# Kernel optimization log

Measured on AMD Instinct MI355X. Metric: run time of the kernel, lower is better.

## Reference

```python
import jax, jax.numpy as jnp
import numpy as np

V = 50000
D = 128
EF = 16
E = 800000
LN_EPS = 1e-5


def setup_inputs() -> dict:
    key = jax.random.key(0)
    ks = jax.random.split(key, 9)
    h = jax.random.normal(ks[0], (V, D), dtype=jnp.float32)
    edge_index = jax.random.randint(ks[1], (2, E), 0, V, dtype=jnp.int64)
    edge_attr = jax.random.normal(ks[2], (E, EF), dtype=jnp.float32)
    # msg_mlp = Linear(D+EF, D) -> ReLU -> Dropout(0) -> Linear(D, D)
    s1 = 1.0 / np.sqrt(D + EF)
    s2 = 1.0 / np.sqrt(D)
    W1 = jax.random.uniform(ks[3], (D + EF, D), minval=-s1, maxval=s1, dtype=jnp.float32)
    b1 = jax.random.uniform(ks[4], (D,), minval=-s1, maxval=s1, dtype=jnp.float32)
    W2 = jax.random.uniform(ks[5], (D, D), minval=-s2, maxval=s2, dtype=jnp.float32)
    b2 = jax.random.uniform(ks[6], (D,), minval=-s2, maxval=s2, dtype=jnp.float32)
    gamma = jnp.ones((D,), dtype=jnp.float32)
    beta = jnp.zeros((D,), dtype=jnp.float32)
    return {"h": h, "edge_index": edge_index, "edge_attr": edge_attr,
            "W1": W1, "b1": b1, "W2": W2, "b2": b2,
            "gamma": gamma, "beta": beta}


def _layer_norm(x, gamma, beta):
    mu = jnp.mean(x, axis=-1, keepdims=True)
    var = jnp.mean(jnp.square(x - mu), axis=-1, keepdims=True)
    return (x - mu) * jax.lax.rsqrt(var + LN_EPS) * gamma + beta


def reference(h, edge_index, edge_attr, W1, b1, W2, b2, gamma, beta):
    src, dst = edge_index[0], edge_index[1]
    # gather source node features, concat edge features: [E, D+EF]
    x = jnp.concatenate([h[src], edge_attr], axis=-1)
    # per-edge message MLP (dropout p=0 -> identity)
    msg = jax.nn.relu(x @ W1 + b1) @ W2 + b2  # [E, D]
    # scatter-add messages to destinations
    agg = jax.ops.segment_sum(msg, dst, num_segments=V)  # [V, D]
    # count initialized to ones BEFORE scatter_add -> denominator = 1 + in_degree
    deg = jax.ops.segment_sum(jnp.ones((E,), dtype=h.dtype), dst, num_segments=V)
    count = (1.0 + deg)[:, None]  # [V, 1]
    return _layer_norm(h + agg / count, gamma, beta)
```

## Files before the change

### kernel.cpp

```cpp
#include <hip/hip_runtime.h>
#include <hip/hip_bf16.h>

#define V 50000
#define D 128
#define EF 16
#define E_EDGES 800000
#define NT 12500
#define XSTR 168
#define YSTR 136
#define CSTR 132
#define NSCAN 196
#define EGRID 1024

typedef __attribute__((ext_vector_type(8))) __bf16 bf16x8;
typedef __attribute__((ext_vector_type(4))) float f32x4;

__device__ inline unsigned short f2bf(float f) {
    unsigned u = __float_as_uint(f);
    u += 0x7FFF + ((u >> 16) & 1);
    return (unsigned short)(u >> 16);
}
__device__ inline unsigned pack2(float a, float b) {
    return (unsigned)f2bf(a) | ((unsigned)f2bf(b) << 16);
}

__global__ __launch_bounds__(256)
void setup_kernel(const float* __restrict__ h, unsigned short* __restrict__ hbf,
                  const int* __restrict__ ei, int* __restrict__ cnt,
                  float* __restrict__ agg,
                  const float* __restrict__ W1, const float* __restrict__ W2,
                  unsigned short* __restrict__ W1p, unsigned short* __restrict__ W2p) {
    int idx = blockIdx.x * 256 + threadIdx.x;
    const float4 v = *(const float4*)(h + ((size_t)idx << 2));
    unsigned* o = (unsigned*)hbf + (idx << 1);
    o[0] = pack2(v.x, v.y);
    o[1] = pack2(v.z, v.w);
    *(float4*)(agg + ((size_t)idx << 2)) = (float4){0.f, 0.f, 0.f, 0.f};
    if (idx < E_EDGES) atomicAdd(&cnt[ei[E_EDGES + idx]], 1);
    if (idx < 5 * 128 * 32) {
        int kb = idx >> 12, rem = idx & 4095;
        int n = rem >> 5, kk = rem & 31;
        int k = kb * 32 + kk;
        W1p[idx] = f2bf((k < D + EF) ? W1[k * D + n] : 0.0f);
    }
    if (idx < 4 * 128 * 32) {
        int kb = idx >> 12, rem = idx & 4095;
        int n = rem >> 5, kk = rem & 31;
        W2p[idx] = f2bf(W2[(kb * 32 + kk) * D + n]);
    }
}

__device__ inline int block_excl_scan(int x, int t, int* ws) {
    int lane = t & 63, w = t >> 6;
    int inc = x;
    #pragma unroll
    for (int off = 1; off < 64; off <<= 1) {
        int y = __shfl_up(inc, off);
        if (lane >= off) inc += y;
    }
    if (lane == 63) ws[w] = inc;
    __syncthreads();
    if (t == 0) {
        int r = 0;
        #pragma unroll
        for (int i = 0; i < 4; ++i) { int c = ws[i]; ws[i] = r; r += c; }
    }
    __syncthreads();
    return inc - x + ws[w];
}

__global__ __launch_bounds__(256)
void scan1_kernel(const int* __restrict__ cnt, int* __restrict__ cursor,
                  int* __restrict__ bsum) {
    __shared__ int ws[4];
    __shared__ int tot;
    int t = threadIdx.x;
    int i = blockIdx.x * 256 + t;
    int x = (i < V) ? cnt[i] : 0;
    int ex = block_excl_scan(x, t, ws);
    if (i < V) cursor[i] = ex;
    if (t == 255) tot = ex + x;
    __syncthreads();
    if (t == 0) bsum[blockIdx.x] = tot;
}

__global__ __launch_bounds__(256)
void scatter_kernel(const int* __restrict__ ei, int* __restrict__ cursor,
                    const int* __restrict__ bsum,
                    int* __restrict__ srcs, int* __restrict__ dsts,
                    int* __restrict__ eidx) {
    __shared__ int ws[4];
    __shared__ int sboff[NSCAN];
    int t = threadIdx.x;
    int x = (t < NSCAN) ? bsum[t] : 0;
    int ex = block_excl_scan(x, t, ws);
    if (t < NSCAN) sboff[t] = ex;
    __syncthreads();
    int e = blockIdx.x * 256 + t;
    int d = ei[E_EDGES + e];
    int pos = atomicAdd(&cursor[d], 1) + sboff[d >> 8];
    srcs[pos] = ei[e];
    dsts[pos] = d;
    eidx[pos] = e;
}

__global__ __launch_bounds__(256, 3)
void edge_kernel(const unsigned short* __restrict__ hbf,
                 const float* __restrict__ ea,
                 const int* __restrict__ srcs, const int* __restrict__ dsts,
                 const int* __restrict__ eidx,
                 const unsigned short* __restrict__ W1p, const unsigned short* __restrict__ W2p,
                 const float* __restrict__ b1, const float* __restrict__ b2,
                 float* __restrict__ agg) {
    union SharedU {
        struct { unsigned short Xs[64 * XSTR]; unsigned short Ys[64 * YSTR]; } s;
        float C[64 * CSTR];
    };
    __shared__ __align__(16) SharedU u;
    __shared__ int sDst[64];

    const int tid  = threadIdx.x;
    const int lane = tid & 63;
    const int wave = tid >> 6;
    const int nlo  = lane & 15;
    const int kq   = lane >> 4;
    const int er   = tid >> 4;
    const int ec   = tid & 15;
    const int ee   = tid >> 2;
    const int eq   = tid & 3;

    bf16x8 B1[5][2], B2[4][2];
    float b1v[2], b2v[2];
    #pragma unroll
    for (int t = 0; t < 2; ++t) {
        int n = wave * 32 + t * 16 + nlo;
        b1v[t] = b1[n];
        b2v[t] = b2[n];
        #pragma unroll
        for (int kb = 0; kb < 5; ++kb)
            B1[kb][t] = *(const bf16x8*)(W1p + ((kb << 7) + n) * 32 + (kq << 3));
        #pragma unroll
        for (int kb = 0; kb < 4; ++kb)
            B2[kb][t] = *(const bf16x8*)(W2p + ((kb << 7) + n) * 32 + (kq << 3));
    }

    const int base0 = blockIdx.x << 6;
    int a0 = srcs[base0 + er];
    int a1 = srcs[base0 + er + 16];
    int a2 = srcs[base0 + er + 32];
    int a3 = srcs[base0 + er + 48];
    int aev = eidx[base0 + ee];
    int ddcur = dsts[base0 + lane];
    bf16x8 pf0 = *(const bf16x8*)(hbf + (size_t)a0 * D + (ec << 3));
    bf16x8 pf1 = *(const bf16x8*)(hbf + (size_t)a1 * D + (ec << 3));
    bf16x8 pf2 = *(const bf16x8*)(hbf + (size_t)a2 * D + (ec << 3));
    bf16x8 pf3 = *(const bf16x8*)(hbf + (size_t)a3 * D + (ec << 3));
    float4 pfe = *(const float4*)(ea + (size_t)aev * EF + (eq << 2));

    int n1 = blockIdx.x + EGRID;
    int nb1 = (n1 < NT ? n1 : blockIdx.x) << 6;
    int i1s0 = srcs[nb1 + er];
    int i1s1 = srcs[nb1 + er + 16];
    int i1s2 = srcs[nb1 + er + 32];
    int i1s3 = srcs[nb1 + er + 48];
    int i1e  = eidx[nb1 + ee];
    int i1d  = dsts[nb1 + lane];

    for (int tile = blockIdx.x; tile < NT; tile += EGRID) {
        int n2 = tile + 2 * EGRID;
        int nb2 = (n2 < NT ? n2 : tile) << 6;
        int i2s0 = srcs[nb2 + er];
        int i2s1 = srcs[nb2 + er + 16];
        int i2s2 = srcs[nb2 + er + 32];
        int i2s3 = srcs[nb2 + er + 48];
        int i2e  = eidx[nb2 + ee];
        int i2d  = dsts[nb2 + lane];

        if (tid < 64) sDst[tid] = ddcur;
        *(bf16x8*)(u.s.Xs + er * XSTR + (ec << 3))        = pf0;
        *(bf16x8*)(u.s.Xs + (er + 16) * XSTR + (ec << 3)) = pf1;
        *(bf16x8*)(u.s.Xs + (er + 32) * XSTR + (ec << 3)) = pf2;
        *(bf16x8*)(u.s.Xs + (er + 48) * XSTR + (ec << 3)) = pf3;
        {
            unsigned* xp = (unsigned*)(u.s.Xs) + ee * (XSTR / 2) + 64 + (eq << 1);
            xp[0] = pack2(pfe.x, pfe.y);
            xp[1] = pack2(pfe.z, pfe.w);
        }
        {
            int i0 = tid, i1 = tid + 256;
            ((unsigned*)(u.s.Xs))[(i0 >> 3) * (XSTR / 2) + 72 + (i0 & 7)] = 0u;
            ((unsigned*)(u.s.Xs))[(i1 >> 3) * (XSTR / 2) + 72 + (i1 & 7)] = 0u;
        }
        __syncthreads();

        bf16x8 q0 = *(const bf16x8*)(hbf + (size_t)i1s0 * D + (ec << 3));
        bf16x8 q1 = *(const bf16x8*)(hbf + (size_t)i1s1 * D + (ec << 3));
        bf16x8 q2 = *(const bf16x8*)(hbf + (size_t)i1s2 * D + (ec << 3));
        bf16x8 q3 = *(const bf16x8*)(hbf + (size_t)i1s3 * D + (ec << 3));
        float4 qe = *(const float4*)(ea + (size_t)i1e * EF + (eq << 2));
        int nextdd = i1d;

        f32x4 acc[4][2];
        #pragma unroll
        for (int mt = 0; mt < 4; ++mt)
            #pragma unroll
            for (int t = 0; t < 2; ++t)
                acc[mt][t] = (f32x4){0.f, 0.f, 0.f, 0.f};

        #pragma unroll
        for (int kb = 0; kb < 5; ++kb) {
            bf16x8 A[4];
            int ko = kb * 32 + (kq << 3);
            #pragma unroll
            for (int mt = 0; mt < 4; ++mt)
                A[mt] = *(const bf16x8*)(u.s.Xs + (mt * 16 + nlo) * XSTR + ko);
            #pragma unroll
            for (int mt = 0; mt < 4; ++mt)
                #pragma unroll
                for (int t = 0; t < 2; ++t)
                    acc[mt][t] = __builtin_amdgcn_mfma_f32_16x16x32_bf16(A[mt], B1[kb][t], acc[mt][t], 0, 0, 0);
        }

        #pragma unroll
        for (int mt = 0; mt < 4; ++mt)
            #pragma unroll
            for (int t = 0; t < 2; ++t)
                #pragma unroll
                for (int r = 0; r < 4; ++r) {
                    float v = fmaxf(acc[mt][t][r] + b1v[t], 0.0f);
                    int row = mt * 16 + (kq << 2) + r;
                    int col = wave * 32 + t * 16 + nlo;
                    u.s.Ys[row * YSTR + col] = f2bf(v);
                }
        __syncthreads();

        f32x4 acc2[4][2];
        #pragma unroll
        for (int mt = 0; mt < 4; ++mt)
            #pragma unroll
            for (int t = 0; t < 2; ++t)
                acc2[mt][t] = (f32x4){0.f, 0.f, 0.f, 0.f};

        #pragma unroll
        for (int kb = 0; kb < 4; ++kb) {
            bf16x8 A[4];
            int ko = kb * 32 + (kq << 3);
            #pragma unroll
            for (int mt = 0; mt < 4; ++mt)
                A[mt] = *(const bf16x8*)(u.s.Ys + (mt * 16 + nlo) * YSTR + ko);
            #pragma unroll
            for (int mt = 0; mt < 4; ++mt)
                #pragma unroll
                for (int t = 0; t < 2; ++t)
                    acc2[mt][t] = __builtin_amdgcn_mfma_f32_16x16x32_bf16(A[mt], B2[kb][t], acc2[mt][t], 0, 0, 0);
        }
        __syncthreads();

        #pragma unroll
        for (int mt = 0; mt < 4; ++mt)
            #pragma unroll
            for (int t = 0; t < 2; ++t)
                #pragma unroll
                for (int r = 0; r < 4; ++r) {
                    int row = mt * 16 + (kq << 2) + r;
                    int col = wave * 32 + t * 16 + nlo;
                    u.C[row * CSTR + col] = acc2[mt][t][r] + b2v[t];
                }
        __syncthreads();

        {
            int col = tid & 127;
            int rbase = (tid >> 7) << 5;
            float sum = 0.f;
            int cur = sDst[rbase];
            for (int i = 0; i < 32; ++i) {
                int row = rbase + i;
                int d = sDst[row];
                if (d != cur) {
                    atomicAdd(&agg[(size_t)cur * D + col], sum);
                    sum = 0.f;
                    cur = d;
                }
                sum += u.C[row * CSTR + col];
            }
            atomicAdd(&agg[(size_t)cur * D + col], sum);
        }
        __syncthreads();

        pf0 = q0; pf1 = q1; pf2 = q2; pf3 = q3; pfe = qe; ddcur = nextdd;
        i1s0 = i2s0; i1s1 = i2s1; i1s2 = i2s2; i1s3 = i2s3; i1e = i2e; i1d = i2d;
    }
}

__global__ __launch_bounds__(256)
void finalize_kernel(const float* __restrict__ h, const float* __restrict__ agg,
                     const int* __restrict__ cnt,
                     const float* __restrict__ gamma, const float* __restrict__ beta,
                     float* __restrict__ out) {
    int wave = threadIdx.x >> 6, lane = threadIdx.x & 63;
    int v = blockIdx.x * 4 + wave;
    if (v >= V) return;
    float inv = 1.0f / (1.0f + (float)cnt[v]);
    const float* hr = h + (size_t)v * D;
    const float* ar = agg + (size_t)v * D;
    float x0 = hr[lane]      + ar[lane]      * inv;
    float x1 = hr[lane + 64] + ar[lane + 64] * inv;
    float s = x0 + x1;
    #pragma unroll
    for (int m = 32; m; m >>= 1) s += __shfl_xor(s, m);
    float mu = s * (1.0f / 128.0f);
    float d0 = x0 - mu, d1 = x1 - mu;
    float vs = d0 * d0 + d1 * d1;
    #pragma unroll
    for (int m = 32; m; m >>= 1) vs += __shfl_xor(vs, m);
    float rs = rsqrtf(vs * (1.0f / 128.0f) + 1e-5f);
    out[(size_t)v * D + lane]      = d0 * rs * gamma[lane]      + beta[lane];
    out[(size_t)v * D + 64 + lane] = d1 * rs * gamma[lane + 64] + beta[lane + 64];
}

extern "C" void kernel_launch(void* const* d_in, const int* in_sizes, int n_in,
                              void* d_out, int out_size, void* d_ws, size_t ws_size,
                              hipStream_t stream) {
    const float* h     = (const float*)d_in[0];
    const int*   ei    = (const int*)d_in[1];
    const float* ea    = (const float*)d_in[2];
    const float* W1    = (const float*)d_in[3];
    const float* b1    = (const float*)d_in[4];
    const float* W2    = (const float*)d_in[5];
    const float* b2    = (const float*)d_in[6];
    const float* gamma = (const float*)d_in[7];
    const float* beta  = (const float*)d_in[8];
    float* out = (float*)d_out;

    char* ws = (char*)d_ws;
    float*          agg    = (float*)ws;
    int*            cnt    = (int*)(ws + 25600000);
    int*            cursor = (int*)(ws + 25800000);
    int*            bsum   = (int*)(ws + 26000000);
    int*            srcs   = (int*)(ws + 26000800);
    int*            dsts   = (int*)(ws + 29200800);
    int*            eidx   = (int*)(ws + 32400800);
    unsigned short* W1p    = (unsigned short*)(ws + 35600800);
    unsigned short* W2p    = (unsigned short*)(ws + 35641760);
    unsigned short* hbf    = (unsigned short*)(ws + 35674528);

    hipMemsetAsync(cnt, 0, 200000, stream);
    setup_kernel<<<6250, 256, 0, stream>>>(h, hbf, ei, cnt, agg, W1, W2, W1p, W2p);
    scan1_kernel<<<NSCAN, 256, 0, stream>>>(cnt, cursor, bsum);
    scatter_kernel<<<3125, 256, 0, stream>>>(ei, cursor, bsum, srcs, dsts, eidx);
    edge_kernel<<<EGRID, 256, 0, stream>>>(hbf, ea, srcs, dsts, eidx, W1p, W2p, b1, b2, agg);
    finalize_kernel<<<12500, 256, 0, stream>>>(h, agg, cnt, gamma, beta, out);
}
```

Before: 376.1 us.

## Precompute per-node h@W1 once and gather projected rows per edge

Uses linearity to compute U = h @ W1[:128] once per node (50k rows) in a new GEMM kernel instead of once per edge (800k), so each edge only computes the small edge-feature part (K=32) and adds the gathered U row before ReLU. This removes most of the first-layer MFMA work and shrinks the shared staging buffer, allowing occupancy to rise from 3 to 4 blocks per CU. The cost is an extra kernel launch plus a bf16 rounding of U before adding the edge term, which changes numerics slightly.

New measurement: 319.8 us. 1.18x faster.

```diff
diff --git a/kernel.cpp b/kernel.cpp
--- a/kernel.cpp
+++ b/kernel.cpp
@@ -6,11 +6,12 @@
 #define EF 16
 #define E_EDGES 800000
 #define NT 12500
-#define XSTR 168
-#define YSTR 136
+#define USTR 136
+#define XESTR 40
 #define CSTR 132
 #define NSCAN 196
 #define EGRID 1024
+#define UGRID 782
 
 typedef __attribute__((ext_vector_type(8))) __bf16 bf16x8;
 typedef __attribute__((ext_vector_type(4))) float f32x4;
@@ -23,18 +24,16 @@
 __device__ inline unsigned pack2(float a, float b) {
     return (unsigned)f2bf(a) | ((unsigned)f2bf(b) << 16);
 }
+__device__ inline float bf2f(unsigned short u) {
+    return __uint_as_float((unsigned)u << 16);
+}
 
 __global__ __launch_bounds__(256)
-void setup_kernel(const float* __restrict__ h, unsigned short* __restrict__ hbf,
-                  const int* __restrict__ ei, int* __restrict__ cnt,
+void setup_kernel(const int* __restrict__ ei, int* __restrict__ cnt,
                   float* __restrict__ agg,
                   const float* __restrict__ W1, const float* __restrict__ W2,
                   unsigned short* __restrict__ W1p, unsigned short* __restrict__ W2p) {
     int idx = blockIdx.x * 256 + threadIdx.x;
-    const float4 v = *(const float4*)(h + ((size_t)idx << 2));
-    unsigned* o = (unsigned*)hbf + (idx << 1);
-    o[0] = pack2(v.x, v.y);
-    o[1] = pack2(v.z, v.w);
     *(float4*)(agg + ((size_t)idx << 2)) = (float4){0.f, 0.f, 0.f, 0.f};
     if (idx < E_EDGES) atomicAdd(&cnt[ei[E_EDGES + idx]], 1);
     if (idx < 5 * 128 * 32) {
@@ -48,6 +47,80 @@
         int n = rem >> 5, kk = rem & 31;
         W2p[idx] = f2bf(W2[(kb * 32 + kk) * D + n]);
     }
+}
+
+__global__ __launch_bounds__(256)
+void u_gemm_kernel(const float* __restrict__ h,
+                   const unsigned short* __restrict__ W1p,
+                   unsigned short* __restrict__ U) {
+    __shared__ __align__(16) unsigned short Hs[64 * USTR];
+    const int tid  = threadIdx.x;
+    const int lane = tid & 63;
+    const int wave = tid >> 6;
+    const int nlo  = lane & 15;
+    const int kq   = lane >> 4;
+    const int er   = tid >> 4;
+    const int ec   = tid & 15;
+    const int gbase = blockIdx.x << 6;
+
+    bf16x8 B1[4][2];
+    #pragma unroll
+    for (int t = 0; t < 2; ++t) {
+        int n = wave * 32 + t * 16 + nlo;
+        #pragma unroll
+        for (int kb = 0; kb < 4; ++kb)
+            B1[kb][t] = *(const bf16x8*)(W1p + ((kb << 7) + n) * 32 + (kq << 3));
+    }
+
+    #pragma unroll
+    for (int m = 0; m < 4; ++m) {
+        int row = er + m * 16;
+        int grow = gbase + row;
+        unsigned* o = (unsigned*)(Hs + row * USTR + (ec << 3));
+        if (grow < V) {
+            const float4* p = (const float4*)(h + (size_t)grow * D + (ec << 3));
+            float4 v0 = p[0], v1 = p[1];
+            o[0] = pack2(v0.x, v0.y); o[1] = pack2(v0.z, v0.w);
+            o[2] = pack2(v1.x, v1.y); o[3] = pack2(v1.z, v1.w);
+        } else {
+            o[0] = 0u; o[1] = 0u; o[2] = 0u; o[3] = 0u;
+        }
+    }
+    __syncthreads();
+
+    f32x4 acc[4][2];
+    #pragma unroll
+    for (int mt = 0; mt < 4; ++mt)
+        #pragma unroll
+        for (int t = 0; t < 2; ++t)
+            acc[mt][t] = (f32x4){0.f, 0.f, 0.f, 0.f};
+
+    #pragma unroll
+    for (int kb = 0; kb < 4; ++kb) {
+        bf16x8 A[4];
+        int ko = kb * 32 + (kq << 3);
+        #pragma unroll
+        for (int mt = 0; mt < 4; ++mt)
+            A[mt] = *(const bf16x8*)(Hs + (mt * 16 + nlo) * USTR + ko);
+        #pragma unroll
+        for (int mt = 0; mt < 4; ++mt)
+            #pragma unroll
+            for (int t = 0; t < 2; ++t)
+                acc[mt][t] = __builtin_amdgcn_mfma_f32_16x16x32_bf16(A[mt], B1[kb][t], acc[mt][t], 0, 0, 0);
+    }
+
+    #pragma unroll
+    for (int mt = 0; mt < 4; ++mt)
+        #pragma unroll
+        for (int t = 0; t < 2; ++t)
+            #pragma unroll
+            for (int r = 0; r < 4; ++r) {
+                int row = mt * 16 + (kq << 2) + r;
+                int grow = gbase + row;
+                int col = wave * 32 + t * 16 + nlo;
+                if (grow < V)
+                    U[(size_t)grow * D + col] = f2bf(acc[mt][t][r]);
+            }
 }
 
 __device__ inline int block_excl_scan(int x, int t, int* ws) {
@@ -104,8 +177,8 @@
     eidx[pos] = e;
 }
 
-__global__ __launch_bounds__(256, 3)
-void edge_kernel(const unsigned short* __restrict__ hbf,
+__global__ __launch_bounds__(256, 4)
+void edge_kernel(const unsigned short* __restrict__ U,
                  const float* __restrict__ ea,
                  const int* __restrict__ srcs, const int* __restrict__ dsts,
                  const int* __restrict__ eidx,
@@ -113,10 +186,11 @@
                  const float* __restrict__ b1, const float* __restrict__ b2,
                  float* __restrict__ agg) {
     union SharedU {
-        struct { unsigned short Xs[64 * XSTR]; unsigned short Ys[64 * YSTR]; } s;
+        unsigned short Us[64 * USTR];
         float C[64 * CSTR];
     };
     __shared__ __align__(16) SharedU u;
+    __shared__ __align__(16) unsigned short Xe[64 * XESTR];
     __shared__ int sDst[64];
 
     const int tid  = threadIdx.x;
@@ -129,19 +203,24 @@
     const int ee   = tid >> 2;
     const int eq   = tid & 3;
 
-    bf16x8 B1[5][2], B2[4][2];
+    bf16x8 B1e[2], B2[4][2];
     float b1v[2], b2v[2];
     #pragma unroll
     for (int t = 0; t < 2; ++t) {
         int n = wave * 32 + t * 16 + nlo;
         b1v[t] = b1[n];
         b2v[t] = b2[n];
-        #pragma unroll
-        for (int kb = 0; kb < 5; ++kb)
-            B1[kb][t] = *(const bf16x8*)(W1p + ((kb << 7) + n) * 32 + (kq << 3));
+        B1e[t] = *(const bf16x8*)(W1p + ((4 << 7) + n) * 32 + (kq << 3));
         #pragma unroll
         for (int kb = 0; kb < 4; ++kb)
             B2[kb][t] = *(const bf16x8*)(W2p + ((kb << 7) + n) * 32 + (kq << 3));
+    }
+
+    {
+        unsigned* xz = (unsigned*)Xe;
+        int i0 = tid, i1 = tid + 256;
+        xz[(i0 >> 3) * (XESTR / 2) + 8 + (i0 & 7)] = 0u;
+        xz[(i1 >> 3) * (XESTR / 2) + 8 + (i1 & 7)] = 0u;
     }
 
     const int base0 = blockIdx.x << 6;
@@ -151,10 +230,10 @@
     int a3 = srcs[base0 + er + 48];
     int aev = eidx[base0 + ee];
     int ddcur = dsts[base0 + lane];
-    bf16x8 pf0 = *(const bf16x8*)(hbf + (size_t)a0 * D + (ec << 3));
-    bf16x8 pf1 = *(const bf16x8*)(hbf + (size_t)a1 * D + (ec << 3));
-    bf16x8 pf2 = *(const bf16x8*)(hbf + (size_t)a2 * D + (ec << 3));
-    bf16x8 pf3 = *(const bf16x8*)(hbf + (size_t)a3 * D + (ec << 3));
+    bf16x8 pf0 = *(const bf16x8*)(U + (size_t)a0 * D + (ec << 3));
+    bf16x8 pf1 = *(const bf16x8*)(U + (size_t)a1 * D + (ec << 3));
+    bf16x8 pf2 = *(const bf16x8*)(U + (size_t)a2 * D + (ec << 3));
+    bf16x8 pf3 = *(const bf16x8*)(U + (size_t)a3 * D + (ec << 3));
     float4 pfe = *(const float4*)(ea + (size_t)aev * EF + (eq << 2));
 
     int n1 = blockIdx.x + EGRID;
@@ -177,48 +256,40 @@
         int i2d  = dsts[nb2 + lane];
 
         if (tid < 64) sDst[tid] = ddcur;
-        *(bf16x8*)(u.s.Xs + er * XSTR + (ec << 3))        = pf0;
-        *(bf16x8*)(u.s.Xs + (er + 16) * XSTR + (ec << 3)) = pf1;
-        *(bf16x8*)(u.s.Xs + (er + 32) * XSTR + (ec << 3)) = pf2;
-        *(bf16x8*)(u.s.Xs + (er + 48) * XSTR + (ec << 3)) = pf3;
+        *(bf16x8*)(u.Us + er * USTR + (ec << 3))        = pf0;
+        *(bf16x8*)(u.Us + (er + 16) * USTR + (ec << 3)) = pf1;
+        *(bf16x8*)(u.Us + (er + 32) * USTR + (ec << 3)) = pf2;
+        *(bf16x8*)(u.Us + (er + 48) * USTR + (ec << 3)) = pf3;
         {
-            unsigned* xp = (unsigned*)(u.s.Xs) + ee * (XSTR / 2) + 64 + (eq << 1);
+            unsigned* xp = (unsigned*)Xe + ee * (XESTR / 2) + (eq << 1);
             xp[0] = pack2(pfe.x, pfe.y);
             xp[1] = pack2(pfe.z, pfe.w);
         }
-        {
-            int i0 = tid, i1 = tid + 256;
-            ((unsigned*)(u.s.Xs))[(i0 >> 3) * (XSTR / 2) + 72 + (i0 & 7)] = 0u;
-            ((unsigned*)(u.s.Xs))[(i1 >> 3) * (XSTR / 2) + 72 + (i1 & 7)] = 0u;
-        }
         __syncthreads();
 
-        bf16x8 q0 = *(const bf16x8*)(hbf + (size_t)i1s0 * D + (ec << 3));
-        bf16x8 q1 = *(const bf16x8*)(hbf + (size_t)i1s1 * D + (ec << 3));
-        bf16x8 q2 = *(const bf16x8*)(hbf + (size_t)i1s2 * D + (ec << 3));
-        bf16x8 q3 = *(const bf16x8*)(hbf + (size_t)i1s3 * D + (ec << 3));
+        bf16x8 q0 = *(const bf16x8*)(U + (size_t)i1s0 * D + (ec << 3));
+        bf16x8 q1 = *(const bf16x8*)(U + (size_t)i1s1 * D + (ec << 3));
+        bf16x8 q2 = *(const bf16x8*)(U + (size_t)i1s2 * D + (ec << 3));
+        bf16x8 q3 = *(const bf16x8*)(U + (size_t)i1s3 * D + (ec << 3));
         float4 qe = *(const float4*)(ea + (size_t)i1e * EF + (eq << 2));
         int nextdd = i1d;
 
-        f32x4 acc[4][2];
+        f32x4 accE[4][2];
         #pragma unroll
         for (int mt = 0; mt < 4; ++mt)
             #pragma unroll
             for (int t = 0; t < 2; ++t)
-                acc[mt][t] = (f32x4){0.f, 0.f, 0.f, 0.f};
-
-        #pragma unroll
-        for (int kb = 0; kb < 5; ++kb) {
+                accE[mt][t] = (f32x4){0.f, 0.f, 0.f, 0.f};
+        {
             bf16x8 A[4];
-            int ko = kb * 32 + (kq << 3);
             #pragma unroll
             for (int mt = 0; mt < 4; ++mt)
-                A[mt] = *(const bf16x8*)(u.s.Xs + (mt * 16 + nlo) * XSTR + ko);
+                A[mt] = *(const bf16x8*)(Xe + (mt * 16 + nlo) * XESTR + (kq << 3));
             #pragma unroll
             for (int mt = 0; mt < 4; ++mt)
                 #pragma unroll
                 for (int t = 0; t < 2; ++t)
-                    acc[mt][t] = __builtin_amdgcn_mfma_f32_16x16x32_bf16(A[mt], B1[kb][t], acc[mt][t], 0, 0, 0);
+                    accE[mt][t] = __builtin_amdgcn_mfma_f32_16x16x32_bf16(A[mt], B1e[t], accE[mt][t], 0, 0, 0);
         }
 
         #pragma unroll
@@ -227,10 +298,11 @@
             for (int t = 0; t < 2; ++t)
                 #pragma unroll
                 for (int r = 0; r < 4; ++r) {
-                    float v = fmaxf(acc[mt][t][r] + b1v[t], 0.0f);
                     int row = mt * 16 + (kq << 2) + r;
                     int col = wave * 32 + t * 16 + nlo;
-                    u.s.Ys[row * YSTR + col] = f2bf(v);
+                    unsigned short* yp = u.Us + row * USTR + col;
+                    float y = fmaxf(bf2f(*yp) + accE[mt][t][r] + b1v[t], 0.0f);
+                    *yp = f2bf(y);
                 }
         __syncthreads();
 
@@ -247,7 +319,7 @@
             int ko = kb * 32 + (kq << 3);
             #pragma unroll
             for (int mt = 0; mt < 4; ++mt)
-                A[mt] = *(const bf16x8*)(u.s.Ys + (mt * 16 + nlo) * YSTR + ko);
+                A[mt] = *(const bf16x8*)(u.Us + (mt * 16 + nlo) * USTR + ko);
             #pragma unroll
             for (int mt = 0; mt < 4; ++mt)
                 #pragma unroll
@@ -342,12 +414,13 @@
     int*            eidx   = (int*)(ws + 32400800);
     unsigned short* W1p    = (unsigned short*)(ws + 35600800);
     unsigned short* W2p    = (unsigned short*)(ws + 35641760);
-    unsigned short* hbf    = (unsigned short*)(ws + 35674528);
+    unsigned short* U      = (unsigned short*)(ws + 35674528);
 
     hipMemsetAsync(cnt, 0, 200000, stream);
-    setup_kernel<<<6250, 256, 0, stream>>>(h, hbf, ei, cnt, agg, W1, W2, W1p, W2p);
+    setup_kernel<<<6250, 256, 0, stream>>>(ei, cnt, agg, W1, W2, W1p, W2p);
+    u_gemm_kernel<<<UGRID, 256, 0, stream>>>(h, W1p, U);
     scan1_kernel<<<NSCAN, 256, 0, stream>>>(cnt, cursor, bsum);
     scatter_kernel<<<3125, 256, 0, stream>>>(ei, cursor, bsum, srcs, dsts, eidx);
-    edge_kernel<<<EGRID, 256, 0, stream>>>(hbf, ea, srcs, dsts, eidx, W1p, W2p, b1, b2, agg);
+    edge_kernel<<<EGRID, 256, 0, stream>>>(U, ea, srcs, dsts, eidx, W1p, W2p, b1, b2, agg);
     finalize_kernel<<<12500, 256, 0, stream>>>(h, agg, cnt, gamma, beta, out);
 }
```
